# Performance work log

Measured on AMD Instinct MI355X. Metric: run time of the kernel, lower is better.

Reference implementation:

```python
import jax, jax.numpy as jnp
import numpy as np

B, N, D = 2, 2048, 1024
H, ENC = 16, 8
HD = D // H
EPS = 1e-5


def _apply_rope(x, cos, sin):
    # x: [B,N,H,HD], cos/sin: [N,HD//2]
    c = cos[None, :, None, :]
    s = sin[None, :, None, :]
    x_re = x[..., 0::2]
    x_im = x[..., 1::2]
    out = jnp.stack([x_re * c - x_im * s, x_re * s + x_im * c], axis=-1)
    return out.reshape(x.shape)


def _rmsnorm(x):
    return x * jax.lax.rsqrt(jnp.mean(x * x, axis=-1, keepdims=True) + EPS)


def setup_inputs() -> dict:
    key = jax.random.key(0)
    ks = jax.random.split(key, 8)
    pos = jnp.arange(N, dtype=jnp.float32)[:, None]
    inv_freq = 1.0 / (10000.0 ** (jnp.arange(0, HD, 2, dtype=jnp.float32) / HD))  # [HD//2]
    ang = pos * inv_freq[None, :]
    std = 0.02
    return {
        "x": jax.random.normal(ks[0], (B, N, D), dtype=jnp.float32),
        "rope_cos": jnp.cos(ang),
        "rope_sin": jnp.sin(ang),
        "Wq": std * jax.random.normal(ks[1], (D, D), dtype=jnp.float32),
        "Wk": std * jax.random.normal(ks[2], (D, D), dtype=jnp.float32),
        "Wv": std * jax.random.normal(ks[3], (D, D), dtype=jnp.float32),
        "Wo_enc": std * jax.random.normal(ks[4], (H * HD, D), dtype=jnp.float32),
        "Wo_dec": std * jax.random.normal(ks[5], ((H - ENC) * HD, D), dtype=jnp.float32),
        "heads": H,
        "encoder_heads": ENC,
    }


def reference(x, rope_cos, rope_sin, Wq, Wk, Wv, Wo_enc, Wo_dec, heads, encoder_heads):
    b, n, d = x.shape
    hd = d // heads
    scale = hd ** (-0.5)
    q = (x @ Wq).reshape(b, n, heads, hd)
    k = (x @ Wk).reshape(b, n, heads, hd)
    v = (x @ Wv).reshape(b, n, heads, hd)
    q = _rmsnorm(_apply_rope(q, rope_cos, rope_sin))
    k = _rmsnorm(_apply_rope(k, rope_cos, rope_sin))
    # scores: [B,H,N,N]
    scores = jnp.einsum("bihd,bjhd->bhij", q, k) * scale
    causal = jnp.tril(jnp.ones((n, n), dtype=bool))  # [N,N]
    is_enc = (jnp.arange(heads) < encoder_heads)[:, None, None]  # [H,1,1]
    allow = jnp.logical_or(is_enc, causal[None, :, :])  # [H,N,N]
    scores = jnp.where(allow[None], scores, -jnp.inf)
    att = jax.nn.softmax(scores, axis=-1)
    out = jnp.einsum("bhij,bjhd->bihd", att, v)  # [B,N,H,HD]
    enc_out = out.reshape(b, n, heads * hd) @ Wo_enc
    dec_out = out[:, :, encoder_heads:, :].reshape(b, n, (heads - encoder_heads) * hd) @ Wo_dec
    return (enc_out, dec_out)
```

## Files before the change

### kernel.cpp

```cpp
#include <hip/hip_runtime.h>
#include <hip/hip_bf16.h>
#include <math.h>

#define B_    2
#define N_    2048
#define D_    1024
#define H_    16
#define ENC_  8
#define HD_   64
#define EPS_  1e-5f
#define M_    (B_ * N_)

typedef __bf16 bf16x8 __attribute__((ext_vector_type(8)));
typedef float  f32x4  __attribute__((ext_vector_type(4)));

#define MB(x) ((size_t)(x) * 1024 * 1024)

__device__ __forceinline__ void gld16(const __bf16* g, __bf16* l) {
    __builtin_amdgcn_global_load_lds(
        (const __attribute__((address_space(1))) void*)g,
        (__attribute__((address_space(3))) void*)l,
        16, 0, 0);
}

template <typename OutT>
__device__ __forceinline__ void gemm_core(
    const __bf16* __restrict__ A, const __bf16* __restrict__ Bt,
    OutT* __restrict__ C, int K, int lda, int aoff, int ldc,
    int bm, int bn, __bf16* As, __bf16* Bs)
{
    const int tid  = threadIdx.x;
    const int w    = tid >> 6;
    const int lane = tid & 63;
    const int lrow = lane & 15;
    const int quad = lane >> 4;
    const int wr   = w >> 1;
    const int wc   = w & 1;

    const int sr = lane >> 2;
    const int sc = (lane & 3) * 8;
    const __bf16* Ag0 = A  + (size_t)(bm +      w * 16 + sr) * lda + aoff + sc;
    const __bf16* Ag1 = A  + (size_t)(bm + 64 + w * 16 + sr) * lda + aoff + sc;
    const __bf16* Bg0 = Bt + (size_t)(bn +      w * 16 + sr) * K + sc;
    const __bf16* Bg1 = Bt + (size_t)(bn + 64 + w * 16 + sr) * K + sc;
    __bf16* Al0 = &As[w * 512];
    __bf16* Al1 = &As[2048 + w * 512];
    __bf16* Bl0 = &Bs[w * 512];
    __bf16* Bl1 = &Bs[2048 + w * 512];

    f32x4 acc[4][4];
    #pragma unroll
    for (int i = 0; i < 4; ++i)
        #pragma unroll
        for (int j = 0; j < 4; ++j) acc[i][j] = (f32x4){0.f, 0.f, 0.f, 0.f};

    for (int k0 = 0; k0 < K; k0 += 32) {
        gld16(Ag0 + k0, Al0);
        gld16(Ag1 + k0, Al1);
        gld16(Bg0 + k0, Bl0);
        gld16(Bg1 + k0, Bl1);
        __syncthreads();

        bf16x8 af[4], bf[4];
        #pragma unroll
        for (int rt = 0; rt < 4; ++rt)
            af[rt] = *(const bf16x8*)&As[(wr * 64 + rt * 16 + lrow) * 32 + quad * 8];
        #pragma unroll
        for (int ct = 0; ct < 4; ++ct)
            bf[ct] = *(const bf16x8*)&Bs[(wc * 64 + ct * 16 + lrow) * 32 + quad * 8];

        #pragma unroll
        for (int rt = 0; rt < 4; ++rt)
            #pragma unroll
            for (int ct = 0; ct < 4; ++ct)
                acc[rt][ct] = __builtin_amdgcn_mfma_f32_16x16x32_bf16(
                    af[rt], bf[ct], acc[rt][ct], 0, 0, 0);
        __syncthreads();
    }

    #pragma unroll
    for (int rt = 0; rt < 4; ++rt)
        #pragma unroll
        for (int ct = 0; ct < 4; ++ct)
            #pragma unroll
            for (int r = 0; r < 4; ++r) {
                const int row = bm + wr * 64 + rt * 16 + quad * 4 + r;
                const int col = bn + wc * 64 + ct * 16 + lrow;
                C[(size_t)row * ldc + col] = (OutT)acc[rt][ct][r];
            }
}

__global__ __launch_bounds__(256) void gemm_qkv(
    const __bf16* __restrict__ A, const __bf16* __restrict__ Bt,
    __bf16* __restrict__ C)
{
    __shared__ __bf16 As[128 * 32];
    __shared__ __bf16 Bs[128 * 32];
    gemm_core<__bf16>(A, Bt, C, D_, D_, 0, 3072,
                      blockIdx.y * 128, blockIdx.x * 128, As, Bs);
}

__global__ __launch_bounds__(256) void gemm_out(
    const __bf16* __restrict__ A, const __bf16* __restrict__ Woe,
    const __bf16* __restrict__ Wod, float* __restrict__ Cenc,
    float* __restrict__ Cdec)
{
    __shared__ __bf16 As[128 * 32];
    __shared__ __bf16 Bs[128 * 32];
    const int bx = blockIdx.x;
    if (bx < 8) {
        gemm_core<float>(A, Woe, Cenc, 1024, D_, 0, D_,
                         blockIdx.y * 128, bx * 128, As, Bs);
    } else {
        gemm_core<float>(A, Wod, Cdec, 512, D_, 512, D_,
                         blockIdx.y * 128, (bx - 8) * 128, As, Bs);
    }
}

__global__ __launch_bounds__(256) void f32_to_bf16(
    const float* __restrict__ src, __bf16* __restrict__ dst)
{
    const size_t i = ((size_t)blockIdx.x * 256 + threadIdx.x) * 8;
    float4 a = *(const float4*)&src[i];
    float4 b = *(const float4*)&src[i + 4];
    bf16x8 o = {(__bf16)a.x, (__bf16)a.y, (__bf16)a.z, (__bf16)a.w,
                (__bf16)b.x, (__bf16)b.y, (__bf16)b.z, (__bf16)b.w};
    *(bf16x8*)&dst[i] = o;
}

struct WtArgs {
    const float* W[5];
    __bf16*      Wt[5];
    int          K[5];
    int          nyb[5];
};

__global__ __launch_bounds__(256) void wt_conv_all(WtArgs a)
{
    const int z = blockIdx.z;
    if (blockIdx.y >= a.nyb[z]) return;
    const float* W  = a.W[z];
    __bf16*      Wt = a.Wt[z];
    const int    K  = a.K[z];

    __shared__ __bf16 t[64][72];
    const int kb = blockIdx.y * 64;
    const int nb = blockIdx.x * 64;
    {
        const int kl = threadIdx.x >> 2;
        const int c0 = (threadIdx.x & 3) * 16;
        const float* src = W + (size_t)(kb + kl) * D_ + nb + c0;
        #pragma unroll
        for (int u = 0; u < 4; ++u) {
            float4 f = *(const float4*)&src[u * 4];
            t[c0 + u * 4 + 0][kl] = (__bf16)f.x;
            t[c0 + u * 4 + 1][kl] = (__bf16)f.y;
            t[c0 + u * 4 + 2][kl] = (__bf16)f.z;
            t[c0 + u * 4 + 3][kl] = (__bf16)f.w;
        }
    }
    __syncthreads();
    {
        const int nl  = threadIdx.x >> 2;
        const int k0c = (threadIdx.x & 3) * 16;
        __bf16* dst = Wt + (size_t)(nb + nl) * K + kb + k0c;
        *(bf16x8*)&dst[0] = *(const bf16x8*)&t[nl][k0c];
        *(bf16x8*)&dst[8] = *(const bf16x8*)&t[nl][k0c + 8];
    }
}

__global__ __launch_bounds__(256) void rope_vconv(
    const __bf16* __restrict__ qkv,
    const float* __restrict__ cs, const float* __restrict__ sn,
    __bf16* __restrict__ qbf, __bf16* __restrict__ kbf,
    __bf16* __restrict__ vt)
{
    if (blockIdx.x < 16384) {
        const int row  = blockIdx.x * 4 + (threadIdx.x >> 6);
        const int lane = threadIdx.x & 63;
        const int n    = (row >> 4) & (N_ - 1);
        const int b    = row >> 15;
        const int h    = row & 15;
        const int p    = lane >> 1;

        const float c = cs[n * (HD_ / 2) + p];
        const float s = sn[n * (HD_ / 2) + p];
        const size_t ibase = (size_t)(b * N_ + n) * 3072 + h * HD_ + lane;
        const size_t obase = ((size_t)(b * H_ + h) * N_ + n) * HD_ + lane;
        const bool odd = (lane & 1);

        {
            float val = (float)qkv[ibase];
            float partner = __shfl_xor(val, 1, 64);
            float r = odd ? fmaf(partner, s, val * c)
                          : (val * c - partner * s);
            float ss = r * r;
            #pragma unroll
            for (int off = 1; off < 64; off <<= 1) ss += __shfl_xor(ss, off, 64);
            qbf[obase] = (__bf16)(r * rsqrtf(ss * (1.0f / 64.0f) + EPS_));
        }
        {
            float val = (float)qkv[ibase + 1024];
            float partner = __shfl_xor(val, 1, 64);
            float r = odd ? fmaf(partner, s, val * c)
                          : (val * c - partner * s);
            float ss = r * r;
            #pragma unroll
            for (int off = 1; off < 64; off <<= 1) ss += __shfl_xor(ss, off, 64);
            kbf[obase] = (__bf16)(r * rsqrtf(ss * (1.0f / 64.0f) + EPS_));
        }
    } else {
        __shared__ __bf16 tile[64][72];
        const int bx = blockIdx.x - 16384;
        const int bh = bx >> 5;
        const int b  = bh >> 4, h = bh & 15;
        const int n0 = (bx & 31) * 64;
        {
            const int nl = threadIdx.x >> 2;
            const int d0 = (threadIdx.x & 3) * 16;
            const __bf16* src =
                qkv + (size_t)(b * N_ + n0 + nl) * 3072 + 2048 + h * HD_ + d0;
            bf16x8 v0 = *(const bf16x8*)&src[0];
            bf16x8 v1 = *(const bf16x8*)&src[8];
            #pragma unroll
            for (int e = 0; e < 8; ++e) {
                tile[d0 + e][nl]     = v0[e];
                tile[d0 + 8 + e][nl] = v1[e];
            }
        }
        __syncthreads();
        {
            const int dl = threadIdx.x >> 2;
            const int nc = (threadIdx.x & 3) * 16;
            __bf16* dst = vt + ((size_t)(bh * HD_ + dl)) * N_ + n0 + nc;
            *(bf16x8*)&dst[0] = *(const bf16x8*)&tile[dl][nc];
            *(bf16x8*)&dst[8] = *(const bf16x8*)&tile[dl][nc + 8];
        }
    }
}

__global__ __launch_bounds__(256) void attn_mfma(
    const __bf16* __restrict__ qbf, const __bf16* __restrict__ kbf,
    const __bf16* __restrict__ vtbf, __bf16* __restrict__ o)
{
    __shared__ __bf16 Ks[2][4096];
    __shared__ __bf16 Vs[2][4096];
    __shared__ __bf16 Plds[4][16][36];

    const int tid  = threadIdx.x;
    const int w    = tid >> 6;
    const int lane = tid & 63;
    const int lrow = lane & 15;
    const int quad = lane >> 4;

    const int bh = blockIdx.x;
    const int qb = gridDim.y - 1 - blockIdx.y;
    const int b  = bh >> 4, h = bh & 15;
    const bool enc = (h < ENC_);
    const int i0 = qb * 64 + w * 16;

    const __bf16* qbase = qbf  + (size_t)bh * N_ * HD_;
    const __bf16* kbase = kbf  + (size_t)bh * N_ * HD_;
    const __bf16* vbase = vtbf + (size_t)bh * HD_ * N_;

    const __bf16* kg0 = kbase + (size_t)lane * HD_ + w * 8;
    const __bf16* kg1 = kbase + (size_t)lane * HD_ + (w + 4) * 8;
    const __bf16* vg  = vbase + (size_t)lane * N_;

    bf16x8 qf[2];
    #pragma unroll
    for (int kc = 0; kc < 2; ++kc)
        qf[kc] = *(const bf16x8*)
            &qbase[(size_t)(i0 + lrow) * HD_ + kc * 32 + quad * 8];

    const f32x4 zero = {0.f, 0.f, 0.f, 0.f};
    f32x4 oacc[4];
    #pragma unroll
    for (int c = 0; c < 4; ++c) oacc[c] = zero;
    float lsum[4] = {};

    const float KSc = 0.125f * 1.4426950408889634f;
    const float KOc = -8.0f  * 1.4426950408889634f;

    const int ntiles = enc ? (N_ >> 6) : (qb + 1);
    const bool dec = !enc;

    auto stage = [&](int t, int bb) {
        const int j0 = t << 6;
        gld16(kg0 + (size_t)j0 * HD_, &Ks[bb][(w)     * 512]);
        gld16(kg1 + (size_t)j0 * HD_, &Ks[bb][(w + 4) * 512]);
        gld16(vg + j0 + w * 8,        &Vs[bb][(w)     * 512]);
        gld16(vg + j0 + (w + 4) * 8,  &Vs[bb][(w + 4) * 512]);
    };

    stage(0, 0);
    for (int t = 0; t < ntiles; ++t) {
        const int bb = t & 1;
        __syncthreads();
        if (t + 1 < ntiles) stage(t + 1, bb ^ 1);

        #pragma unroll
        for (int s = 0; s < 2; ++s) {
            const int jp = (t << 6) + s * 32;

            bf16x8 kf0 = *(const bf16x8*)&Ks[bb][((quad)     * 64 + s * 32 + lrow) * 8];
            bf16x8 kf1 = *(const bf16x8*)&Ks[bb][((4 + quad) * 64 + s * 32 + lrow) * 8];
            bf16x8 kf2 = *(const bf16x8*)&Ks[bb][((quad)     * 64 + s * 32 + 16 + lrow) * 8];
            bf16x8 kf3 = *(const bf16x8*)&Ks[bb][((4 + quad) * 64 + s * 32 + 16 + lrow) * 8];

            f32x4 s0 = zero, s1 = zero;
            s0 = __builtin_amdgcn_mfma_f32_16x16x32_bf16(qf[0], kf0, s0, 0, 0, 0);
            s0 = __builtin_amdgcn_mfma_f32_16x16x32_bf16(qf[1], kf1, s0, 0, 0, 0);
            s1 = __builtin_amdgcn_mfma_f32_16x16x32_bf16(qf[0], kf2, s1, 0, 0, 0);
            s1 = __builtin_amdgcn_mfma_f32_16x16x32_bf16(qf[1], kf3, s1, 0, 0, 0);

            if (dec && (jp + 31 > i0)) {
                #pragma unroll
                for (int r = 0; r < 4; ++r) {
                    const int i  = i0 + quad * 4 + r;
                    float pA = (jp + lrow      <= i) ? exp2f(fmaf(s0[r], KSc, KOc)) : 0.f;
                    float pB = (jp + 16 + lrow <= i) ? exp2f(fmaf(s1[r], KSc, KOc)) : 0.f;
                    lsum[r] += pA + pB;
                    Plds[w][quad * 4 + r][lrow]      = (__bf16)pA;
                    Plds[w][quad * 4 + r][lrow + 16] = (__bf16)pB;
                }
            } else {
                #pragma unroll
                for (int r = 0; r < 4; ++r) {
                    float pA = exp2f(fmaf(s0[r], KSc, KOc));
                    float pB = exp2f(fmaf(s1[r], KSc, KOc));
                    lsum[r] += pA + pB;
                    Plds[w][quad * 4 + r][lrow]      = (__bf16)pA;
                    Plds[w][quad * 4 + r][lrow + 16] = (__bf16)pB;
                }
            }

            bf16x8 vf0 = *(const bf16x8*)&Vs[bb][((s * 4 + quad) * 64 +  0 + lrow) * 8];
            bf16x8 vf1 = *(const bf16x8*)&Vs[bb][((s * 4 + quad) * 64 + 16 + lrow) * 8];
            bf16x8 vf2 = *(const bf16x8*)&Vs[bb][((s * 4 + quad) * 64 + 32 + lrow) * 8];
            bf16x8 vf3 = *(const bf16x8*)&Vs[bb][((s * 4 + quad) * 64 + 48 + lrow) * 8];

            bf16x8 pf = *(const bf16x8*)&Plds[w][lrow][quad * 8];
            oacc[0] = __builtin_amdgcn_mfma_f32_16x16x32_bf16(pf, vf0, oacc[0], 0, 0, 0);
            oacc[1] = __builtin_amdgcn_mfma_f32_16x16x32_bf16(pf, vf1, oacc[1], 0, 0, 0);
            oacc[2] = __builtin_amdgcn_mfma_f32_16x16x32_bf16(pf, vf2, oacc[2], 0, 0, 0);
            oacc[3] = __builtin_amdgcn_mfma_f32_16x16x32_bf16(pf, vf3, oacc[3], 0, 0, 0);
        }
    }

    #pragma unroll
    for (int r = 0; r < 4; ++r) {
        float s = lsum[r];
        s += __shfl_xor(s, 1, 64);
        s += __shfl_xor(s, 2, 64);
        s += __shfl_xor(s, 4, 64);
        s += __shfl_xor(s, 8, 64);
        lsum[r] = 1.0f / s;
    }

    #pragma unroll
    for (int c = 0; c < 4; ++c)
        #pragma unroll
        for (int r = 0; r < 4; ++r) {
            const int i = i0 + quad * 4 + r;
            o[(size_t)(b * N_ + i) * D_ + h * HD_ + c * 16 + lrow] =
                (__bf16)(oacc[c][r] * lsum[r]);
        }
}

extern "C" void kernel_launch(void* const* d_in, const int* in_sizes, int n_in,
                              void* d_out, int out_size, void* d_ws, size_t ws_size,
                              hipStream_t stream)
{
    const float* x   = (const float*)d_in[0];
    const float* cs  = (const float*)d_in[1];
    const float* sn  = (const float*)d_in[2];
    const float* Wq  = (const float*)d_in[3];
    const float* Wk  = (const float*)d_in[4];
    const float* Wv  = (const float*)d_in[5];
    const float* Woe = (const float*)d_in[6];
    const float* Wod = (const float*)d_in[7];

    float* enc_out = (float*)d_out;
    float* dec_out = enc_out + (size_t)M_ * D_;

    char* ws = (char*)d_ws;
    __bf16* xbf    = (__bf16*)(ws);
    __bf16* wqkv_t = (__bf16*)(ws + MB(8));
    __bf16* woe_t  = (__bf16*)(ws + MB(14));
    __bf16* wod_t  = (__bf16*)(ws + MB(16));
    __bf16* qkv    = (__bf16*)(ws + MB(17));
    __bf16* qbf    = (__bf16*)(ws + MB(41));
    __bf16* kbf    = (__bf16*)(ws + MB(49));
    __bf16* vtbf   = xbf;
    __bf16* obuf   = qkv;

    f32_to_bf16<<<(M_ * D_) / (256 * 8), 256, 0, stream>>>(x, xbf);

    WtArgs wa;
    wa.W[0] = Wq;  wa.Wt[0] = wqkv_t;                 wa.K[0] = 1024; wa.nyb[0] = 16;
    wa.W[1] = Wk;  wa.Wt[1] = wqkv_t + 1024 * 1024;   wa.K[1] = 1024; wa.nyb[1] = 16;
    wa.W[2] = Wv;  wa.Wt[2] = wqkv_t + 2048 * 1024;   wa.K[2] = 1024; wa.nyb[2] = 16;
    wa.W[3] = Woe; wa.Wt[3] = woe_t;                  wa.K[3] = 1024; wa.nyb[3] = 16;
    wa.W[4] = Wod; wa.Wt[4] = wod_t;                  wa.K[4] = 512;  wa.nyb[4] = 8;
    wt_conv_all<<<dim3(16, 16, 5), 256, 0, stream>>>(wa);

    gemm_qkv<<<dim3(3072 / 128, M_ / 128), 256, 0, stream>>>(xbf, wqkv_t, qkv);

    rope_vconv<<<16384 + 1024, 256, 0, stream>>>(qkv, cs, sn, qbf, kbf, vtbf);

    attn_mfma<<<dim3(B_ * H_, N_ / 64), 256, 0, stream>>>(qbf, kbf, vtbf, obuf);

    gemm_out<<<dim3(16, M_ / 128), 256, 0, stream>>>(
        obuf, woe_t, wod_t, enc_out, dec_out);
}
```

Measured before the change: 251.7 us.

## Balance causal attention by pairing decoder query blocks and permuting V layout

The attention grid becomes a flat 768-block launch. Encoder heads keep one query block per CTA, while each decoder CTA processes two complementary causal query blocks (31-p and p), so every decoder CTA does roughly the same amount of work. The V transpose now writes columns in an interleaved order, which lets each lane store its two P values as a single packed bf16x2 LDS write instead of two scalar writes. The cost is fewer, longer decoder CTAs and an extra barrier between the two work items.

```diff
diff --git a/kernel.cpp b/kernel.cpp
--- a/kernel.cpp
+++ b/kernel.cpp
@@ -12,6 +12,7 @@
 #define M_    (B_ * N_)
 
 typedef __bf16 bf16x8 __attribute__((ext_vector_type(8)));
+typedef __bf16 bf16x2 __attribute__((ext_vector_type(2)));
 typedef float  f32x4  __attribute__((ext_vector_type(4)));
 
 #define MB(x) ((size_t)(x) * 1024 * 1024)
@@ -233,8 +234,16 @@
             const int dl = threadIdx.x >> 2;
             const int nc = (threadIdx.x & 3) * 16;
             __bf16* dst = vt + ((size_t)(bh * HD_ + dl)) * N_ + n0 + nc;
-            *(bf16x8*)&dst[0] = *(const bf16x8*)&tile[dl][nc];
-            *(bf16x8*)&dst[8] = *(const bf16x8*)&tile[dl][nc + 8];
+            bf16x8 o0, o1;
+            #pragma unroll
+            for (int e = 0; e < 8; ++e) {
+                const int p0 = nc + e;
+                const int p1 = nc + 8 + e;
+                o0[e] = tile[dl][(p0 & ~31) + ((p0 & 31) >> 1) + 16 * (p0 & 1)];
+                o1[e] = tile[dl][(p1 & ~31) + ((p1 & 31) >> 1) + 16 * (p1 & 1)];
+            }
+            *(bf16x8*)&dst[0] = o0;
+            *(bf16x8*)&dst[8] = o1;
         }
     }
 }
@@ -253,11 +262,25 @@
     const int lrow = lane & 15;
     const int quad = lane >> 4;
 
-    const int bh = blockIdx.x;
-    const int qb = gridDim.y - 1 - blockIdx.y;
-    const int b  = bh >> 4, h = bh & 15;
+    int bh, nwork, qbs[2];
+    if (blockIdx.x < 512) {
+        const int e = blockIdx.x >> 5;
+        bh = (e >> 3) * 16 + (e & 7);
+        qbs[0] = blockIdx.x & 31;
+        qbs[1] = 0;
+        nwork = 1;
+    } else {
+        const int idx = blockIdx.x - 512;
+        const int e = idx >> 4;
+        bh = (e >> 3) * 16 + 8 + (e & 7);
+        const int p = idx & 15;
+        qbs[0] = 31 - p;
+        qbs[1] = p;
+        nwork = 2;
+    }
+    const int b = bh >> 4, h = bh & 15;
     const bool enc = (h < ENC_);
-    const int i0 = qb * 64 + w * 16;
+    const bool dec = !enc;
 
     const __bf16* qbase = qbf  + (size_t)bh * N_ * HD_;
     const __bf16* kbase = kbf  + (size_t)bh * N_ * HD_;
@@ -267,105 +290,109 @@
     const __bf16* kg1 = kbase + (size_t)lane * HD_ + (w + 4) * 8;
     const __bf16* vg  = vbase + (size_t)lane * N_;
 
-    bf16x8 qf[2];
-    #pragma unroll
-    for (int kc = 0; kc < 2; ++kc)
-        qf[kc] = *(const bf16x8*)
-            &qbase[(size_t)(i0 + lrow) * HD_ + kc * 32 + quad * 8];
-
     const f32x4 zero = {0.f, 0.f, 0.f, 0.f};
-    f32x4 oacc[4];
-    #pragma unroll
-    for (int c = 0; c < 4; ++c) oacc[c] = zero;
-    float lsum[4] = {};
-
     const float KSc = 0.125f * 1.4426950408889634f;
     const float KOc = -8.0f  * 1.4426950408889634f;
 
-    const int ntiles = enc ? (N_ >> 6) : (qb + 1);
-    const bool dec = !enc;
-
-    auto stage = [&](int t, int bb) {
-        const int j0 = t << 6;
-        gld16(kg0 + (size_t)j0 * HD_, &Ks[bb][(w)     * 512]);
-        gld16(kg1 + (size_t)j0 * HD_, &Ks[bb][(w + 4) * 512]);
-        gld16(vg + j0 + w * 8,        &Vs[bb][(w)     * 512]);
-        gld16(vg + j0 + (w + 4) * 8,  &Vs[bb][(w + 4) * 512]);
-    };
-
-    stage(0, 0);
-    for (int t = 0; t < ntiles; ++t) {
-        const int bb = t & 1;
-        __syncthreads();
-        if (t + 1 < ntiles) stage(t + 1, bb ^ 1);
-
-        #pragma unroll
-        for (int s = 0; s < 2; ++s) {
-            const int jp = (t << 6) + s * 32;
-
-            bf16x8 kf0 = *(const bf16x8*)&Ks[bb][((quad)     * 64 + s * 32 + lrow) * 8];
-            bf16x8 kf1 = *(const bf16x8*)&Ks[bb][((4 + quad) * 64 + s * 32 + lrow) * 8];
-            bf16x8 kf2 = *(const bf16x8*)&Ks[bb][((quad)     * 64 + s * 32 + 16 + lrow) * 8];
-            bf16x8 kf3 = *(const bf16x8*)&Ks[bb][((4 + quad) * 64 + s * 32 + 16 + lrow) * 8];
-
-            f32x4 s0 = zero, s1 = zero;
-            s0 = __builtin_amdgcn_mfma_f32_16x16x32_bf16(qf[0], kf0, s0, 0, 0, 0);
-            s0 = __builtin_amdgcn_mfma_f32_16x16x32_bf16(qf[1], kf1, s0, 0, 0, 0);
-            s1 = __builtin_amdgcn_mfma_f32_16x16x32_bf16(qf[0], kf2, s1, 0, 0, 0);
-            s1 = __builtin_amdgcn_mfma_f32_16x16x32_bf16(qf[1], kf3, s1, 0, 0, 0);
-
-            if (dec && (jp + 31 > i0)) {
-                #pragma unroll
-                for (int r = 0; r < 4; ++r) {
-                    const int i  = i0 + quad * 4 + r;
-                    float pA = (jp + lrow      <= i) ? exp2f(fmaf(s0[r], KSc, KOc)) : 0.f;
-                    float pB = (jp + 16 + lrow <= i) ? exp2f(fmaf(s1[r], KSc, KOc)) : 0.f;
-                    lsum[r] += pA + pB;
-                    Plds[w][quad * 4 + r][lrow]      = (__bf16)pA;
-                    Plds[w][quad * 4 + r][lrow + 16] = (__bf16)pB;
+    for (int wi = 0; wi < nwork; ++wi) {
+        const int qb = qbs[wi];
+        const int i0 = qb * 64 + w * 16;
+        const int ntiles = enc ? (N_ >> 6) : (qb + 1);
+
+        bf16x8 qf[2];
+        #pragma unroll
+        for (int kc = 0; kc < 2; ++kc)
+            qf[kc] = *(const bf16x8*)
+                &qbase[(size_t)(i0 + lrow) * HD_ + kc * 32 + quad * 8];
+
+        f32x4 oacc[4];
+        #pragma unroll
+        for (int c = 0; c < 4; ++c) oacc[c] = zero;
+        float lsum[4] = {};
+
+        auto stage = [&](int t, int bb) {
+            const int j0 = t << 6;
+            gld16(kg0 + (size_t)j0 * HD_, &Ks[bb][(w)     * 512]);
+            gld16(kg1 + (size_t)j0 * HD_, &Ks[bb][(w + 4) * 512]);
+            gld16(vg + j0 + w * 8,        &Vs[bb][(w)     * 512]);
+            gld16(vg + j0 + (w + 4) * 8,  &Vs[bb][(w + 4) * 512]);
+        };
+
+        if (wi) __syncthreads();
+        stage(0, 0);
+        for (int t = 0; t < ntiles; ++t) {
+            const int bb = t & 1;
+            __syncthreads();
+            if (t + 1 < ntiles) stage(t + 1, bb ^ 1);
+
+            #pragma unroll
+            for (int s = 0; s < 2; ++s) {
+                const int jp = (t << 6) + s * 32;
+
+                bf16x8 kf0 = *(const bf16x8*)&Ks[bb][((quad)     * 64 + s * 32 + lrow) * 8];
+                bf16x8 kf1 = *(const bf16x8*)&Ks[bb][((4 + quad) * 64 + s * 32 + lrow) * 8];
+                bf16x8 kf2 = *(const bf16x8*)&Ks[bb][((quad)     * 64 + s * 32 + 16 + lrow) * 8];
+                bf16x8 kf3 = *(const bf16x8*)&Ks[bb][((4 + quad) * 64 + s * 32 + 16 + lrow) * 8];
+
+                f32x4 s0 = zero, s1 = zero;
+                s0 = __builtin_amdgcn_mfma_f32_16x16x32_bf16(qf[0], kf0, s0, 0, 0, 0);
+                s0 = __builtin_amdgcn_mfma_f32_16x16x32_bf16(qf[1], kf1, s0, 0, 0, 0);
+                s1 = __builtin_amdgcn_mfma_f32_16x16x32_bf16(qf[0], kf2, s1, 0, 0, 0);
+                s1 = __builtin_amdgcn_mfma_f32_16x16x32_bf16(qf[1], kf3, s1, 0, 0, 0);
+
+                if (dec && (jp + 31 > i0)) {
+                    #pragma unroll
+                    for (int r = 0; r < 4; ++r) {
+                        const int i  = i0 + quad * 4 + r;
+                        float pA = (jp + lrow      <= i) ? exp2f(fmaf(s0[r], KSc, KOc)) : 0.f;
+                        float pB = (jp + 16 + lrow <= i) ? exp2f(fmaf(s1[r], KSc, KOc)) : 0.f;
+                        lsum[r] += pA + pB;
+                        bf16x2 pp = {(__bf16)pA, (__bf16)pB};
+                        *(bf16x2*)&Plds[w][quad * 4 + r][2 * lrow] = pp;
+                    }
+                } else {
+                    #pragma unroll
+                    for (int r = 0; r < 4; ++r) {
+                        float pA = exp2f(fmaf(s0[r], KSc, KOc));
+                        float pB = exp2f(fmaf(s1[r], KSc, KOc));
+                        lsum[r] += pA + pB;
+                        bf16x2 pp = {(__bf16)pA, (__bf16)pB};
+                        *(bf16x2*)&Plds[w][quad * 4 + r][2 * lrow] = pp;
+                    }
                 }
-            } else {
-                #pragma unroll
-                for (int r = 0; r < 4; ++r) {
-                    float pA = exp2f(fmaf(s0[r], KSc, KOc));
-                    float pB = exp2f(fmaf(s1[r], KSc, KOc));
-                    lsum[r] += pA + pB;
-                    Plds[w][quad * 4 + r][lrow]      = (__bf16)pA;
-                    Plds[w][quad * 4 + r][lrow + 16] = (__bf16)pB;
-                }
+
+                bf16x8 vf0 = *(const bf16x8*)&Vs[bb][((s * 4 + quad) * 64 +  0 + lrow) * 8];
+                bf16x8 vf1 = *(const bf16x8*)&Vs[bb][((s * 4 + quad) * 64 + 16 + lrow) * 8];
+                bf16x8 vf2 = *(const bf16x8*)&Vs[bb][((s * 4 + quad) * 64 + 32 + lrow) * 8];
+                bf16x8 vf3 = *(const bf16x8*)&Vs[bb][((s * 4 + quad) * 64 + 48 + lrow) * 8];
+
+                bf16x8 pf = *(const bf16x8*)&Plds[w][lrow][quad * 8];
+                oacc[0] = __builtin_amdgcn_mfma_f32_16x16x32_bf16(pf, vf0, oacc[0], 0, 0, 0);
+                oacc[1] = __builtin_amdgcn_mfma_f32_16x16x32_bf16(pf, vf1, oacc[1], 0, 0, 0);
+                oacc[2] = __builtin_amdgcn_mfma_f32_16x16x32_bf16(pf, vf2, oacc[2], 0, 0, 0);
+                oacc[3] = __builtin_amdgcn_mfma_f32_16x16x32_bf16(pf, vf3, oacc[3], 0, 0, 0);
             }
-
-            bf16x8 vf0 = *(const bf16x8*)&Vs[bb][((s * 4 + quad) * 64 +  0 + lrow) * 8];
-            bf16x8 vf1 = *(const bf16x8*)&Vs[bb][((s * 4 + quad) * 64 + 16 + lrow) * 8];
-            bf16x8 vf2 = *(const bf16x8*)&Vs[bb][((s * 4 + quad) * 64 + 32 + lrow) * 8];
-            bf16x8 vf3 = *(const bf16x8*)&Vs[bb][((s * 4 + quad) * 64 + 48 + lrow) * 8];
-
-            bf16x8 pf = *(const bf16x8*)&Plds[w][lrow][quad * 8];
-            oacc[0] = __builtin_amdgcn_mfma_f32_16x16x32_bf16(pf, vf0, oacc[0], 0, 0, 0);
-            oacc[1] = __builtin_amdgcn_mfma_f32_16x16x32_bf16(pf, vf1, oacc[1], 0, 0, 0);
-            oacc[2] = __builtin_amdgcn_mfma_f32_16x16x32_bf16(pf, vf2, oacc[2], 0, 0, 0);
-            oacc[3] = __builtin_amdgcn_mfma_f32_16x16x32_bf16(pf, vf3, oacc[3], 0, 0, 0);
-        }
-    }
-
-    #pragma unroll
-    for (int r = 0; r < 4; ++r) {
-        float s = lsum[r];
-        s += __shfl_xor(s, 1, 64);
-        s += __shfl_xor(s, 2, 64);
-        s += __shfl_xor(s, 4, 64);
-        s += __shfl_xor(s, 8, 64);
-        lsum[r] = 1.0f / s;
-    }
-
-    #pragma unroll
-    for (int c = 0; c < 4; ++c)
+        }
+
         #pragma unroll
         for (int r = 0; r < 4; ++r) {
-            const int i = i0 + quad * 4 + r;
-            o[(size_t)(b * N_ + i) * D_ + h * HD_ + c * 16 + lrow] =
-                (__bf16)(oacc[c][r] * lsum[r]);
-        }
+            float s = lsum[r];
+            s += __shfl_xor(s, 1, 64);
+            s += __shfl_xor(s, 2, 64);
+            s += __shfl_xor(s, 4, 64);
+            s += __shfl_xor(s, 8, 64);
+            lsum[r] = 1.0f / s;
+        }
+
+        #pragma unroll
+        for (int c = 0; c < 4; ++c)
+            #pragma unroll
+            for (int r = 0; r < 4; ++r) {
+                const int i = i0 + quad * 4 + r;
+                o[(size_t)(b * N_ + i) * D_ + h * HD_ + c * 16 + lrow] =
+                    (__bf16)(oacc[c][r] * lsum[r]);
+            }
+    }
 }
 
 extern "C" void kernel_launch(void* const* d_in, const int* in_sizes, int n_in,
@@ -409,7 +436,7 @@
 
     rope_vconv<<<16384 + 1024, 256, 0, stream>>>(qkv, cs, sn, qbf, kbf, vtbf);
 
-    attn_mfma<<<dim3(B_ * H_, N_ / 64), 256, 0, stream>>>(qbf, kbf, vtbf, obuf);
+    attn_mfma<<<dim3(768), 256, 0, stream>>>(qbf, kbf, vtbf, obuf);
 
     gemm_out<<<dim3(16, M_ / 128), 256, 0, stream>>>(
         obuf, woe_t, wod_t, enc_out, dec_out);
```

Result: faster. 238.5 us (-5.3%).
